# Optimization experiments

Measured on AMD Instinct MI355X. Metric: run time of the kernel, lower is better.

## Reference

```python
import jax, jax.numpy as jnp
from jax import lax
import numpy as np

B = 256
# conv stack: (in_ch, out_ch, kernel)
_CONV_CFG = [(1, 3, 4), (3, 9, 4), (9, 12, 4), (12, 15, 4), (15, 15, 3)]
_FLAT = 15 * 4 ** 4  # 3840, matches nn.Linear(15*(18-14)**4, 100)


def _conv4d(x, w, b):
    """True 4D valid convolution. x: [B,C,d1,d2,d3,d4], w: [O,I,k,k,k,k]."""
    dn = lax.conv_dimension_numbers(x.shape, w.shape, ('NCDHWX', 'OIDHWX', 'NCDHWX'))
    y = lax.conv_general_dilated(x, w, window_strides=(1, 1, 1, 1),
                                 padding='VALID', dimension_numbers=dn)
    return y + b.reshape((1, -1) + (1,) * 4)


def setup_inputs() -> dict:
    key = jax.random.key(0)
    ks = jax.random.split(key, 16)
    inp = {'x': jax.random.normal(ks[0], (B, 1, 18, 18, 18, 18), dtype=jnp.float32)}
    for i, (ci, co, k) in enumerate(_CONV_CFG, start=1):
        fan_in = ci * k ** 4
        inp[f'w{i}'] = jax.random.normal(ks[2 * i - 1], (co, ci, k, k, k, k), dtype=jnp.float32) / np.sqrt(fan_in)
        inp[f'b{i}'] = jnp.zeros((co,), dtype=jnp.float32)
    inp['fc1_w'] = jax.random.normal(ks[11], (_FLAT, 100), dtype=jnp.float32) / np.sqrt(_FLAT)
    inp['fc1_b'] = jnp.zeros((100,), dtype=jnp.float32)
    inp['fc2_w'] = jax.random.normal(ks[12], (100, 1), dtype=jnp.float32) / np.sqrt(100.0)
    inp['fc2_b'] = jnp.zeros((1,), dtype=jnp.float32)
    return inp


def reference(x, w1, b1, w2, b2, w3, b3, w4, b4, w5, b5, fc1_w, fc1_b, fc2_w, fc2_b):
    h = jax.nn.relu(_conv4d(x, w1, b1))
    h = jax.nn.relu(_conv4d(h, w2, b2))
    h = jax.nn.relu(_conv4d(h, w3, b3))
    h = jax.nn.relu(_conv4d(h, w4, b4))
    h = jax.nn.relu(_conv4d(h, w5, b5))  # [B,15,4,4,4,4]
    h = h.reshape(h.shape[0], -1)        # [B,3840], torch Flatten order
    # Dropout(0.5) is identity at inference (eval mode)
    h = jax.nn.relu(h @ fc1_w + fc1_b)
    return jax.nn.sigmoid(h @ fc2_w + fc2_b)  # [B,1]
```

## Files before the change

### kernel.cpp

```cpp
#include <hip/hip_runtime.h>
#include <hip/hip_bf16.h>


#define BATCH 256
typedef unsigned int u32;
typedef float    f32x4  __attribute__((ext_vector_type(4)));
typedef float    f32x16 __attribute__((ext_vector_type(16)));
typedef _Float16 f16x8  __attribute__((ext_vector_type(8)));

struct __attribute__((packed, aligned(4))) f16x8w { f16x8 v; };

__global__ void cvt_f32_f16(const float* __restrict__ in, _Float16* __restrict__ o, int n8) {
    int i = blockIdx.x * blockDim.x + threadIdx.x;
    if (i >= n8) return;
    const f32x4* p = (const f32x4*)(in + (size_t)i * 8);
    f32x4 a = p[0], b = p[1];
    f16x8 v;
    #pragma unroll
    for (int j = 0; j < 4; ++j) { v[j] = (_Float16)a[j]; v[4 + j] = (_Float16)b[j]; }
    *(f16x8*)(o + (size_t)i * 8) = v;
}

template<int COUT, int CIN, int KS, int S>
__global__ void prepack_v5(const float* __restrict__ w, _Float16* __restrict__ wf) {
    constexpr int STEPS = CIN * KS * 2 * KS;
    constexpr int TOT = STEPS * 512;
    int idx = blockIdx.x * 256 + threadIdx.x;
    if (idx >= TOT) return;
    int j    = idx & 7;
    int lane = (idx >> 3) & 63;
    int st   = idx >> 9;
    int k1 = st % KS;
    int r1 = st / KS;
    int k3p = r1 & 1;
    int r2  = r1 >> 1;
    int k2 = r2 % KS;
    int ci = r2 / KS;
    int gg = lane >> 5, col = lane & 31;
    int oc = col / S, s = col % S;
    int k3 = k3p * 2 + gg;
    int k4 = j - s;
    float v = 0.0f;
    if (oc < COUT && k3 < KS && k4 >= 0 && k4 < KS)
        v = w[((((oc * CIN + ci) * KS + k1) * KS + k2) * KS + k3) * KS + k4];
    wf[idx] = (_Float16)v;
}

template<int BYTES>
__device__ __forceinline__ void stage_b(const _Float16* gsrc, char* ldst, int tid) {
    constexpr int N16 = BYTES / 16;
    const int wv = tid >> 6, ln = tid & 63;
    #pragma unroll
    for (int it = 0; it * 256 < N16; ++it) {
        int u16 = it * 256 + (wv << 6);
        if (u16 < N16) {
            const char* gp = (const char*)gsrc + (size_t)(u16 + ln) * 16;
            __builtin_amdgcn_global_load_lds(
                (const __attribute__((address_space(1))) unsigned int*)gp,
                (__attribute__((address_space(3))) unsigned int*)(ldst + u16 * 16),
                16, 0, 0);
        }
    }
}

template<int CIN, int COUT, int KS, int DIN, int DP, int S, int OP, int T,
         int CG, int MINW, int SODD, int WSHIFT>
__launch_bounds__(256, MINW)
__global__ void conv4d_v13(const _Float16* __restrict__ x,
                           const _Float16* __restrict__ xs,
                           const _Float16* __restrict__ wf,
                           const float* __restrict__ bias,
                           _Float16* __restrict__ out,
                           _Float16* __restrict__ outs) {
    constexpr int DOUT = DIN - KS + 1;
    constexpr int NB   = (DOUT + S - 1) / S;
    constexpr int PCOL = DOUT * DOUT * NB;
    constexpr int NTC  = (PCOL + 31) / 32;
    constexpr int NG   = DOUT / T;
    static_assert(DOUT % T == 0, "T must divide DOUT");
    constexpr int XD2 = DIN * DP;
    constexpr int XD1 = DIN * XD2;
    constexpr int XCI = DIN * XD1;
    constexpr int GROUPS = CIN * KS * 2;
    static_assert(GROUPS % CG == 0, "CG must divide GROUPS");
    constexpr int CSTEPS = CG * KS;
    constexpr int CBYTES = CSTEPS * 1024;
    constexpr int NCHUNK = GROUPS / CG;
    constexpr int NBUF   = (NCHUNK > 1) ? 2 : 1;
    constexpr int AJ = T + KS - 1;
    constexpr int W  = T + 1;
    constexpr u32 NW   = (u32)BATCH * NG * NTC;
    constexpr u32 POUT = (u32)DOUT * DOUT * DOUT * OP;

    __shared__ char bsm[NBUF * CBYTES];
    const int tid = threadIdx.x;
    u32 wid = blockIdx.x * 4u + (u32)(tid >> 6);
    if (wid >= NW) wid = NW - 1u;
    const int ln = tid & 63;
    const int g  = ln >> 5;
    const int r  = ln & 31;

    u32 tc = wid % (u32)NTC;  u32 q = wid / (u32)NTC;
    u32 d1g = q % (u32)NG;    u32 b = q / (u32)NG;
    u32 rr = tc * 32u + (u32)r;  if (rr >= (u32)PCOL) rr = (u32)PCOL - 1u;
    u32 u  = rr % (u32)NB;    u32 q2 = rr / (u32)NB;
    u32 d3 = q2 % (u32)DOUT;  u32 d2 = q2 / (u32)DOUT;

    const u32 o = b * (u32)(CIN * XCI) + d1g * (u32)(T * XD1)
                + d2 * (u32)XD2 + d3 * (u32)DP + (u32)(g * DP) + u * (u32)S;
    const char* xb;
    if (SODD) {
        u32 p = o & 1u;
        xb = p ? ((const char*)xs + (size_t)(o - 1u) * 2)
               : ((const char*)x  + (size_t)o * 2);
    } else {
        xb = (const char*)x + (size_t)o * 2;
    }

    f32x16 acc[T];
    #pragma unroll
    for (int t = 0; t < T; ++t)
        #pragma unroll
        for (int i = 0; i < 16; ++i) acc[t][i] = 0.0f;

    stage_b<CBYTES>(wf, &bsm[0], tid);

    #pragma unroll 1
    for (int ch = 0; ch < NCHUNK; ++ch) {
        __syncthreads();
        if (NCHUNK > 1 && ch + 1 < NCHUNK)
            stage_b<CBYTES>(wf + (size_t)(ch + 1) * CSTEPS * 512,
                            &bsm[((ch + 1) & 1) * CBYTES], tid);
        const char* bb = &bsm[(ch & 1) * (NBUF > 1 ? CBYTES : 0)] + ln * 16;
        #pragma unroll
        for (int gi = 0; gi < CG; ++gi) {
            int grp = ch * CG + gi;
            int k3p = grp & 1;
            int k2  = (grp >> 1) % KS;
            int ci  = (grp >> 1) / KS;
            u32 goff = ((u32)ci * (u32)XCI + (u32)k2 * (u32)XD2
                      + (u32)(k3p * 2 * DP)) * 2u;
            const char* ap = xb + goff;

            f16x8 ar[W];
            #pragma unroll
            for (int j = 0; j < T; ++j)
                ar[j] = ((const f16x8w*)(ap + j * (XD1 * 2)))->v;
            #pragma unroll
            for (int k1 = 0; k1 < KS; ++k1) {
                if (T + k1 < AJ)
                    ar[(T + k1) % W] = ((const f16x8w*)(ap + (T + k1) * (XD1 * 2)))->v;
                f16x8 bf = *(const f16x8*)(bb + (gi * KS + k1) * 1024);
                #pragma unroll
                for (int t = 0; t < T; ++t)
                    acc[t] = __builtin_amdgcn_mfma_f32_32x32x16_f16(
                        ar[(k1 + t) % W], bf, acc[t], 0, 0, 0);
            }
        }
    }

    const int oc = r / S, s = r % S;
    if (oc >= COUT) return;
    float bv = bias[oc];
    #pragma unroll
    for (int reg = 0; reg < 16; ++reg) {
        int rowoff = (reg & 3) + 8 * (reg >> 2) + 4 * g;
        u32 rr2 = tc * 32u + (u32)rowoff;
        if (rr2 >= (u32)PCOL) rr2 = (u32)PCOL - 1u;
        u32 uu = rr2 % (u32)NB;  u32 qq = rr2 / (u32)NB;
        u32 dd3 = qq % (u32)DOUT; u32 dd2 = qq / (u32)DOUT;
        u32 d4 = uu * (u32)S + (u32)s;
        if (d4 < (u32)DOUT) {
            u32 obase = (b * (u32)COUT + (u32)oc) * POUT
                      + (dd2 * (u32)DOUT + dd3) * (u32)OP + d4
                      + d1g * (u32)(T * DOUT * DOUT * OP);
            #pragma unroll
            for (int t = 0; t < T; ++t) {
                u32 oidx = obase + (u32)t * (u32)(DOUT * DOUT * OP);
                _Float16 v = (_Float16)fmaxf(acc[t][reg] + bv, 0.0f);
                out[oidx] = v;
                if (WSHIFT) { if (oidx >= 1u) outs[oidx - 1u] = v; }
            }
        }
    }
}

__global__ void prepack_fc1(const float* __restrict__ w, _Float16* __restrict__ wf) {
    int idx = blockIdx.x * 256 + threadIdx.x;
    if (idx >= 430080) return;
    int j    = idx & 7;
    int lane = (idx >> 3) & 63;
    int t9   = idx >> 9;
    int st   = t9 % 120;
    int ni   = t9 / 120;
    int k    = st * 32 + (lane >> 4) * 8 + j;
    int col  = ni * 16 + (lane & 15);
    wf[idx] = (_Float16)((col < 100) ? w[k * 100 + col] : 0.0f);
}

__launch_bounds__(256)
__global__ void fc1_mfma(const _Float16* __restrict__ h,
                         const _Float16* __restrict__ wfc,
                         const float* __restrict__ bias,
                         float* __restrict__ o) {
    int wv   = blockIdx.x * 4 + (threadIdx.x >> 6);
    int lane = threadIdx.x & 63;
    int r = lane & 15, g = lane >> 4;
    int mi = wv / 7, ni = wv % 7;
    const f16x8* A  = (const f16x8*)(h + (size_t)(mi * 16 + r) * 3840);
    const f16x8* Bv = (const f16x8*)wfc;
    f32x4 acc = {0.f, 0.f, 0.f, 0.f};
    #pragma unroll 4
    for (int st = 0; st < 120; ++st) {
        f16x8 a = A[st * 4 + g];
        f16x8 b = Bv[(ni * 120 + st) * 64 + lane];
        acc = __builtin_amdgcn_mfma_f32_16x16x32_f16(a, b, acc, 0, 0, 0);
    }
    int col = ni * 16 + r;
    if (col < 100) {
        float bv = bias[col];
        #pragma unroll
        for (int i = 0; i < 4; ++i) {
            int row = mi * 16 + g * 4 + i;
            o[row * 100 + col] = fmaxf(acc[i] + bv, 0.0f);
        }
    }
}

__global__ void fc2_sigmoid(const float* __restrict__ h,
                            const float* __restrict__ w,
                            const float* __restrict__ bias,
                            float* __restrict__ out) {
    int b = blockIdx.x * blockDim.x + threadIdx.x;
    if (b >= BATCH) return;
    const float* hb = h + b * 100;
    float acc = bias[0];
    #pragma unroll
    for (int j = 0; j < 100; ++j)
        acc = fmaf(hb[j], w[j], acc);
    out[b] = 1.0f / (1.0f + expf(-acc));
}

extern "C" void kernel_launch(void* const* d_in, const int* in_sizes, int n_in,
                              void* d_out, int out_size, void* d_ws, size_t ws_size,
                              hipStream_t stream) {
    const float* x    = (const float*)d_in[0];
    const float* w1   = (const float*)d_in[1];
    const float* b1   = (const float*)d_in[2];
    const float* w2   = (const float*)d_in[3];
    const float* b2   = (const float*)d_in[4];
    const float* w3   = (const float*)d_in[5];
    const float* b3   = (const float*)d_in[6];
    const float* w4   = (const float*)d_in[7];
    const float* b4   = (const float*)d_in[8];
    const float* w5   = (const float*)d_in[9];
    const float* b5   = (const float*)d_in[10];
    const float* fc1w = (const float*)d_in[11];
    const float* fc1b = (const float*)d_in[12];
    const float* fc2w = (const float*)d_in[13];
    const float* fc2b = (const float*)d_in[14];
    float* out = (float*)d_out;

    _Float16* W = (_Float16*)d_ws;
    _Float16* x16 = W;
    _Float16* h1  = W + 26873856;
    _Float16* h1s = W + 68345856;
    _Float16* h2  = W + 109817856;
    _Float16* wf1 = W + 157593600;
    _Float16* wf2 = W + 157609984;
    _Float16* wf3 = W + 157659136;
    _Float16* wf4 = W + 157806592;
    _Float16* wf5 = W + 158003200;
    _Float16* wfc = W + 158141440;
    float* fc1out = (float*)(W + 158571520);
    _Float16* h3  = h1s;
    _Float16* h4  = h1s + 22394880;
    _Float16* h5  = h1s + 27371520;

    cvt_f32_f16<<<13122, 256, 0, stream>>>(x, x16, 3359232);

    prepack_v5<3, 1, 4, 4><<<64,  256, 0, stream>>>(w1, wf1);
    prepack_v5<9, 3, 4, 3><<<192, 256, 0, stream>>>(w2, wf2);
    prepack_v5<12, 9, 4, 2><<<576, 256, 0, stream>>>(w3, wf3);
    prepack_v5<15, 12, 4, 2><<<768, 256, 0, stream>>>(w4, wf4);
    prepack_v5<15, 15, 3, 2><<<540, 256, 0, stream>>>(w5, wf5);
    prepack_fc1<<<1680, 256, 0, stream>>>(fc1w, wfc);

    conv4d_v13<1, 3, 4, 18, 18, 4, 16, 3, 8, 4, 0, 1>
        <<<9280, 256, 0, stream>>>(x16, x16, wf1, b1, h1, h1s);
    conv4d_v13<3, 9, 4, 15, 16, 3, 12, 6, 4, 3, 1, 0>
        <<<2304, 256, 0, stream>>>(h1, h1s, wf2, b2, h2, h2);
    conv4d_v13<9, 12, 4, 12, 12, 2, 10, 3, 4, 4, 0, 0>
        <<<2496, 256, 0, stream>>>(h2, h2, wf3, b3, h3, h3);
    conv4d_v13<12, 15, 4, 9, 10, 2, 6, 3, 4, 4, 0, 0>
        <<<512, 256, 0, stream>>>(h3, h3, wf4, b4, h4, h4);
    conv4d_v13<15, 15, 3, 6, 6, 2, 4, 4, 6, 4, 0, 0>
        <<<64, 256, 0, stream>>>(h4, h4, wf5, b5, h5, h5);

    fc1_mfma<<<28, 256, 0, stream>>>(h5, wfc, fc1b, fc1out);
    fc2_sigmoid<<<1, 256, 0, stream>>>(fc1out, fc2w, fc2b, out);
}
```

Measured before the change: 905.9 us.

## Use S=5 column packing for conv1 with shifted fp16 input copy, fuse prepacks, add MFMA priority

The input conversion now also writes a copy of the fp16 input shifted by one element, so conv1 can use an odd-offset source (SODD=1) and pack five d4 positions per output column instead of four. That shrinks the conv1 grid. The six weight-prepack launches are merged into one kernel to cut launch overhead. The conv inner loop also raises wave priority around the MFMA block. The costs are an extra input-sized write and a reshuffled workspace layout in which h2 reuses the x16 region.

```diff
diff --git a/kernel.cpp b/kernel.cpp
--- a/kernel.cpp
+++ b/kernel.cpp
@@ -10,26 +10,29 @@
 
 struct __attribute__((packed, aligned(4))) f16x8w { f16x8 v; };
 
-__global__ void cvt_f32_f16(const float* __restrict__ in, _Float16* __restrict__ o, int n8) {
+__global__ void cvt_f32_f16_pair(const float* __restrict__ in,
+                                 _Float16* __restrict__ o,
+                                 _Float16* __restrict__ os, int n8) {
     int i = blockIdx.x * blockDim.x + threadIdx.x;
     if (i >= n8) return;
     const f32x4* p = (const f32x4*)(in + (size_t)i * 8);
     f32x4 a = p[0], b = p[1];
-    f16x8 v;
+    float c = (i + 1 < n8) ? in[(size_t)i * 8 + 8] : 0.0f;
+    f16x8 v, vs;
     #pragma unroll
     for (int j = 0; j < 4; ++j) { v[j] = (_Float16)a[j]; v[4 + j] = (_Float16)b[j]; }
-    *(f16x8*)(o + (size_t)i * 8) = v;
-}
-
-template<int COUT, int CIN, int KS, int S>
-__global__ void prepack_v5(const float* __restrict__ w, _Float16* __restrict__ wf) {
-    constexpr int STEPS = CIN * KS * 2 * KS;
-    constexpr int TOT = STEPS * 512;
-    int idx = blockIdx.x * 256 + threadIdx.x;
-    if (idx >= TOT) return;
-    int j    = idx & 7;
-    int lane = (idx >> 3) & 63;
-    int st   = idx >> 9;
+    #pragma unroll
+    for (int j = 0; j < 7; ++j) vs[j] = v[j + 1];
+    vs[7] = (_Float16)c;
+    *(f16x8*)(o  + (size_t)i * 8) = v;
+    *(f16x8*)(os + (size_t)i * 8) = vs;
+}
+
+__device__ __forceinline__ _Float16 conv_wf_elem(const float* __restrict__ w,
+        int e, int COUT, int CIN, int KS, int S) {
+    int j    = e & 7;
+    int lane = (e >> 3) & 63;
+    int st   = e >> 9;
     int k1 = st % KS;
     int r1 = st / KS;
     int k3p = r1 & 1;
@@ -43,7 +46,36 @@
     float v = 0.0f;
     if (oc < COUT && k3 < KS && k4 >= 0 && k4 < KS)
         v = w[((((oc * CIN + ci) * KS + k1) * KS + k2) * KS + k3) * KS + k4];
-    wf[idx] = (_Float16)v;
+    return (_Float16)v;
+}
+
+__global__ void prepack_all(const float* __restrict__ w1, const float* __restrict__ w2,
+                            const float* __restrict__ w3, const float* __restrict__ w4,
+                            const float* __restrict__ w5, const float* __restrict__ fw,
+                            _Float16* __restrict__ wf1, _Float16* __restrict__ wf2,
+                            _Float16* __restrict__ wf3, _Float16* __restrict__ wf4,
+                            _Float16* __restrict__ wf5, _Float16* __restrict__ wfc) {
+    int idx = blockIdx.x * 256 + threadIdx.x;
+    if (idx < 16384)  { wf1[idx] = conv_wf_elem(w1, idx, 3, 1, 4, 5);  return; }
+    idx -= 16384;
+    if (idx < 49152)  { wf2[idx] = conv_wf_elem(w2, idx, 9, 3, 4, 3);  return; }
+    idx -= 49152;
+    if (idx < 147456) { wf3[idx] = conv_wf_elem(w3, idx, 12, 9, 4, 2); return; }
+    idx -= 147456;
+    if (idx < 196608) { wf4[idx] = conv_wf_elem(w4, idx, 15, 12, 4, 2); return; }
+    idx -= 196608;
+    if (idx < 138240) { wf5[idx] = conv_wf_elem(w5, idx, 15, 15, 3, 2); return; }
+    idx -= 138240;
+    if (idx < 430080) {
+        int j    = idx & 7;
+        int lane = (idx >> 3) & 63;
+        int t9   = idx >> 9;
+        int st   = t9 % 120;
+        int ni   = t9 / 120;
+        int k    = st * 32 + (lane >> 4) * 8 + j;
+        int col  = ni * 16 + (lane & 15);
+        wfc[idx] = (_Float16)((col < 100) ? fw[k * 100 + col] : 0.0f);
+    }
 }
 
 template<int BYTES>
@@ -66,7 +98,7 @@
 template<int CIN, int COUT, int KS, int DIN, int DP, int S, int OP, int T,
          int CG, int MINW, int SODD, int WSHIFT>
 __launch_bounds__(256, MINW)
-__global__ void conv4d_v13(const _Float16* __restrict__ x,
+__global__ void conv4d_v14(const _Float16* __restrict__ x,
                            const _Float16* __restrict__ xs,
                            const _Float16* __restrict__ wf,
                            const float* __restrict__ bias,
@@ -151,10 +183,12 @@
                 if (T + k1 < AJ)
                     ar[(T + k1) % W] = ((const f16x8w*)(ap + (T + k1) * (XD1 * 2)))->v;
                 f16x8 bf = *(const f16x8*)(bb + (gi * KS + k1) * 1024);
+                __builtin_amdgcn_s_setprio(1);
                 #pragma unroll
                 for (int t = 0; t < T; ++t)
                     acc[t] = __builtin_amdgcn_mfma_f32_32x32x16_f16(
                         ar[(k1 + t) % W], bf, acc[t], 0, 0, 0);
+                __builtin_amdgcn_s_setprio(0);
             }
         }
     }
@@ -185,19 +219,6 @@
     }
 }
 
-__global__ void prepack_fc1(const float* __restrict__ w, _Float16* __restrict__ wf) {
-    int idx = blockIdx.x * 256 + threadIdx.x;
-    if (idx >= 430080) return;
-    int j    = idx & 7;
-    int lane = (idx >> 3) & 63;
-    int t9   = idx >> 9;
-    int st   = t9 % 120;
-    int ni   = t9 / 120;
-    int k    = st * 32 + (lane >> 4) * 8 + j;
-    int col  = ni * 16 + (lane & 15);
-    wf[idx] = (_Float16)((col < 100) ? w[k * 100 + col] : 0.0f);
-}
-
 __launch_bounds__(256)
 __global__ void fc1_mfma(const _Float16* __restrict__ h,
                          const _Float16* __restrict__ wfc,
@@ -262,39 +283,35 @@
     float* out = (float*)d_out;
 
     _Float16* W = (_Float16*)d_ws;
-    _Float16* x16 = W;
-    _Float16* h1  = W + 26873856;
-    _Float16* h1s = W + 68345856;
-    _Float16* h2  = W + 109817856;
-    _Float16* wf1 = W + 157593600;
-    _Float16* wf2 = W + 157609984;
-    _Float16* wf3 = W + 157659136;
-    _Float16* wf4 = W + 157806592;
-    _Float16* wf5 = W + 158003200;
-    _Float16* wfc = W + 158141440;
-    float* fc1out = (float*)(W + 158571520);
-    _Float16* h3  = h1s;
-    _Float16* h4  = h1s + 22394880;
-    _Float16* h5  = h1s + 27371520;
-
-    cvt_f32_f16<<<13122, 256, 0, stream>>>(x, x16, 3359232);
-
-    prepack_v5<3, 1, 4, 4><<<64,  256, 0, stream>>>(w1, wf1);
-    prepack_v5<9, 3, 4, 3><<<192, 256, 0, stream>>>(w2, wf2);
-    prepack_v5<12, 9, 4, 2><<<576, 256, 0, stream>>>(w3, wf3);
-    prepack_v5<15, 12, 4, 2><<<768, 256, 0, stream>>>(w4, wf4);
-    prepack_v5<15, 15, 3, 2><<<540, 256, 0, stream>>>(w5, wf5);
-    prepack_fc1<<<1680, 256, 0, stream>>>(fc1w, wfc);
-
-    conv4d_v13<1, 3, 4, 18, 18, 4, 16, 3, 8, 4, 0, 1>
-        <<<9280, 256, 0, stream>>>(x16, x16, wf1, b1, h1, h1s);
-    conv4d_v13<3, 9, 4, 15, 16, 3, 12, 6, 4, 3, 1, 0>
+    _Float16* x16  = W;
+    _Float16* x16s = W + 26873856;
+    _Float16* h1   = W + 53747712;
+    _Float16* h1s  = W + 95219712;
+    _Float16* h2   = W;
+    _Float16* h3   = h1s;
+    _Float16* h4   = h1s + 22394880;
+    _Float16* h5   = h1s + 27371520;
+    _Float16* wf1  = W + 136691712;
+    _Float16* wf2  = W + 136708096;
+    _Float16* wf3  = W + 136757248;
+    _Float16* wf4  = W + 136904704;
+    _Float16* wf5  = W + 137101312;
+    _Float16* wfc  = W + 137239552;
+    float* fc1out  = (float*)(W + 137669632);
+
+    cvt_f32_f16_pair<<<13122, 256, 0, stream>>>(x, x16, x16s, 3359232);
+    prepack_all<<<3820, 256, 0, stream>>>(w1, w2, w3, w4, w5, fc1w,
+                                          wf1, wf2, wf3, wf4, wf5, wfc);
+
+    conv4d_v14<1, 3, 4, 18, 18, 5, 16, 3, 8, 4, 1, 1>
+        <<<7040, 256, 0, stream>>>(x16, x16s, wf1, b1, h1, h1s);
+    conv4d_v14<3, 9, 4, 15, 16, 3, 12, 6, 4, 3, 1, 0>
         <<<2304, 256, 0, stream>>>(h1, h1s, wf2, b2, h2, h2);
-    conv4d_v13<9, 12, 4, 12, 12, 2, 10, 3, 4, 4, 0, 0>
+    conv4d_v14<9, 12, 4, 12, 12, 2, 10, 3, 4, 4, 0, 0>
         <<<2496, 256, 0, stream>>>(h2, h2, wf3, b3, h3, h3);
-    conv4d_v13<12, 15, 4, 9, 10, 2, 6, 3, 4, 4, 0, 0>
+    conv4d_v14<12, 15, 4, 9, 10, 2, 6, 3, 4, 4, 0, 0>
         <<<512, 256, 0, stream>>>(h3, h3, wf4, b4, h4, h4);
-    conv4d_v13<15, 15, 3, 6, 6, 2, 4, 4, 6, 4, 0, 0>
+    conv4d_v14<15, 15, 3, 6, 6, 2, 4, 4, 6, 4, 0, 0>
         <<<64, 256, 0, stream>>>(h4, h4, wf5, b5, h5, h5);
 
     fc1_mfma<<<28, 256, 0, stream>>>(h5, wfc, fc1b, fc1out);
```

Result: faster. 865.6 us (-4.5%).
